# Kernel optimization log

Hardware: AMD Instinct MI355X
Metric: run time of the kernel (lower is better)

The kernel has to match this reference:

```python
import jax, jax.numpy as jnp
import numpy as np

N_AGENTS, OBS_DIM, HID, ACT_DIM = 8192, 64, 128, 16


def setup_inputs() -> dict:
    key = jax.random.key(0)
    k = jax.random.split(key, 8)
    obs_agents = jax.random.normal(k[0], (N_AGENTS, OBS_DIM), dtype=jnp.float32)
    # binary adjacency, {0,1}, int32 (index/mask semantics, non-differentiable)
    adj = jax.random.randint(k[1], (N_AGENTS, N_AGENTS), 0, 2, dtype=jnp.int32)
    def lin(kk, fan_in, fan_out):
        lim = 1.0 / np.sqrt(fan_in)
        kw, kb = jax.random.split(kk)
        W = jax.random.uniform(kw, (fan_in, fan_out), jnp.float32, -lim, lim)
        b = jax.random.uniform(kb, (fan_out,), jnp.float32, -lim, lim)
        return W, b
    W1, b1 = lin(k[2], OBS_DIM, HID)          # encoder
    W2, b2 = lin(k[3], 2 * HID, HID)          # actor layer 1
    W3, b3 = lin(k[4], HID, ACT_DIM)          # actor layer 2
    return {"obs_agents": obs_agents, "adj": adj,
            "W1": W1, "b1": b1, "W2": W2, "b2": b2, "W3": W3, "b3": b3}


def reference(obs_agents, adj, W1, b1, W2, b2, W3, b3):
    # per-agent encode: h = tanh(obs @ W1 + b1)  -> [N, HID]
    h = jnp.tanh(obs_agents @ W1 + b1)
    # neighbor mean message: mean of h[j] over j with adj[i,j]!=0, zeros if no neighbors
    a = adj.astype(h.dtype)                      # [N, N] binary
    deg = jnp.sum(a, axis=1, keepdims=True)      # [N, 1]
    msg = (a @ h) / jnp.maximum(deg, 1.0)        # zero rows stay zero
    # actor MLP on concat([h, msg])
    combined = jnp.concatenate([h, msg], axis=-1)            # [N, 2*HID]
    hid = jnp.tanh(combined @ W2 + b2)                        # [N, HID]
    logits = hid @ W3 + b3                                    # [N, ACT_DIM]
    return logits
```

## Files before the change

### kernel.cpp

```cpp
#include <hip/hip_runtime.h>
#include <stdint.h>
#include <math.h>

#define NAG 8192
#define NB  144
#define BM  64
#define LDA 72
#define LDB 72
#define NSPLIT 8

typedef __attribute__((ext_vector_type(8))) short short8;
typedef __attribute__((ext_vector_type(4))) float floatx4;

__device__ __forceinline__ float bf2f(unsigned short u) {
    union { uint32_t i; float f; } v; v.i = ((uint32_t)u) << 16; return v.f;
}
__device__ __forceinline__ unsigned short f2bf(float f) {
    union { float f; uint32_t i; } v; v.f = f;
    uint32_t x = v.i;
    return (unsigned short)((x + 0x7FFFu + ((x >> 16) & 1u)) >> 16);
}
__device__ __forceinline__ unsigned short f2h(float f) {
    union { _Float16 h; unsigned short u; } v; v.h = (_Float16)f; return v.u;
}
__device__ __forceinline__ float h2f(unsigned short u) {
    union { _Float16 h; unsigned short u; } v; v.u = u; return (float)v.h;
}

__global__ __launch_bounds__(64) void k0_init(
    int* __restrict__ flag, const unsigned short* __restrict__ W1raw)
{
    int big = 0;
    #pragma unroll
    for (int j = 0; j < 8; ++j) {
        float v = bf2f(W1raw[threadIdx.x * 8 + j]);
        if (!(fabsf(v) <= 1e6f)) big = 1;
    }
    unsigned long long m = __ballot(big);
    if (threadIdx.x == 0) *flag = (m != 0ull) ? 1 : 0;
}

__global__ __launch_bounds__(256) void k1_encode(
    const void* __restrict__ obs,
    const void* __restrict__ W1,
    const void* __restrict__ b1,
    const int* __restrict__ flag,
    float* __restrict__ h_f32,
    unsigned short* __restrict__ hT)
{
    __shared__ float obs_lds[32][68];
    __shared__ unsigned short ht_lds[128][33];
    const int t = threadIdx.x;
    const int abase = blockIdx.x * 32;
    const bool isf = (*flag != 0);

    {
        int a = t >> 3, c0 = (t & 7) * 8;
        if (isf) {
            const float* p = (const float*)obs;
            #pragma unroll
            for (int j = 0; j < 8; ++j)
                obs_lds[a][c0 + j] = p[(size_t)(abase + a) * 64 + c0 + j];
        } else {
            const unsigned short* p = (const unsigned short*)obs;
            #pragma unroll
            for (int j = 0; j < 8; ++j)
                obs_lds[a][c0 + j] = bf2f(p[(size_t)(abase + a) * 64 + c0 + j]);
        }
    }
    __syncthreads();

    const int o = t & 127;
    const int half = t >> 7;
    float acc[16];
    if (isf) {
        const float* Wp = (const float*)W1;
        float bias = ((const float*)b1)[o];
        #pragma unroll
        for (int i = 0; i < 16; ++i) acc[i] = bias;
        for (int k0 = 0; k0 < 64; k0 += 8) {
            float w[8];
            #pragma unroll
            for (int j = 0; j < 8; ++j) w[j] = Wp[(k0 + j) * 128 + o];
            #pragma unroll
            for (int j = 0; j < 8; ++j)
                #pragma unroll
                for (int i = 0; i < 16; ++i)
                    acc[i] = fmaf(obs_lds[half * 16 + i][k0 + j], w[j], acc[i]);
        }
    } else {
        const unsigned short* Wp = (const unsigned short*)W1;
        float bias = bf2f(((const unsigned short*)b1)[o]);
        #pragma unroll
        for (int i = 0; i < 16; ++i) acc[i] = bias;
        for (int k0 = 0; k0 < 64; k0 += 8) {
            float w[8];
            #pragma unroll
            for (int j = 0; j < 8; ++j) w[j] = bf2f(Wp[(k0 + j) * 128 + o]);
            #pragma unroll
            for (int j = 0; j < 8; ++j)
                #pragma unroll
                for (int i = 0; i < 16; ++i)
                    acc[i] = fmaf(obs_lds[half * 16 + i][k0 + j], w[j], acc[i]);
        }
    }
    #pragma unroll
    for (int i = 0; i < 16; ++i) {
        float th = tanhf(acc[i]);
        int a = half * 16 + i;
        h_f32[(size_t)(abase + a) * 128 + o] = th;
        ht_lds[o][a] = f2bf(th);
    }
    __syncthreads();

    for (int p = 0; p < 18; ++p) {
        int n = p * 8 + (t >> 5);
        int a = t & 31;
        unsigned short v;
        if (n < 128)       v = ht_lds[n][a];
        else if (n == 128) v = 0x3F80;
        else               v = 0;
        hT[(size_t)n * NAG + abase + a] = v;
    }
}

__global__ __launch_bounds__(256, 4) void k2_msggemm(
    const int* __restrict__ adj,
    const unsigned short* __restrict__ hT,
    unsigned short* __restrict__ Cp16)
{
    __shared__ __align__(16) unsigned short Alds[BM * LDA];
    __shared__ __align__(16) unsigned short Blds[NB * LDB];
    const int t = threadIdx.x;
    const int mtile = blockIdx.x & 127;
    const int ks = blockIdx.x >> 7;
    const int row0 = mtile * BM;
    const int kbeg = ks * 1024;

    const int wave = t >> 6, lane = t & 63;
    const int fm = lane & 15, quad = lane >> 4;

    floatx4 acc[9];
    #pragma unroll
    for (int i = 0; i < 9; ++i) acc[i] = (floatx4)0.f;

    const int ar = t >> 2, aq = t & 3;
    const int bln = t & 7, brow = t >> 3;

    const int* aP = adj + (size_t)(row0 + ar) * NAG + aq * 16;
    int4 rA0[4], rA1[4];
    uint4 rB[5];

#define LOADA(R, K) do { \
        _Pragma("unroll") \
        for (int c = 0; c < 4; ++c) \
            (R)[c] = *reinterpret_cast<const int4*>(aP + (K) + c * 4); \
    } while (0)
#define LOADB(K) do { \
        _Pragma("unroll") \
        for (int p = 0; p < 5; ++p) { \
            int n = p * 32 + brow; \
            if (n < NB) rB[p] = *reinterpret_cast<const uint4*>(hT + (size_t)n * NAG + (K) + bln * 8); \
        } \
    } while (0)
#define STOREA(R) do { \
        _Pragma("unroll") \
        for (int c = 0; c < 4; ++c) { \
            uint32_t d0 = ((uint32_t)(R)[c].x | ((uint32_t)(R)[c].y << 16)) * 0x3F80u; \
            uint32_t d1 = ((uint32_t)(R)[c].z | ((uint32_t)(R)[c].w << 16)) * 0x3F80u; \
            *reinterpret_cast<uint2*>(&Alds[ar * LDA + aq * 16 + c * 4]) = make_uint2(d0, d1); \
        } \
    } while (0)
#define STOREB() do { \
        _Pragma("unroll") \
        for (int p = 0; p < 5; ++p) { \
            int n = p * 32 + brow; \
            if (n < NB) *reinterpret_cast<uint4*>(&Blds[n * LDB + bln * 8]) = rB[p]; \
        } \
    } while (0)
#define COMPUTE() do { \
        _Pragma("unroll") \
        for (int kk = 0; kk < 64; kk += 32) { \
            short8 af = *reinterpret_cast<const short8*>(&Alds[(wave * 16 + fm) * LDA + kk + quad * 8]); \
            _Pragma("unroll") \
            for (int j = 0; j < 9; ++j) { \
                short8 bf = *reinterpret_cast<const short8*>(&Blds[(j * 16 + fm) * LDB + kk + quad * 8]); \
                acc[j] = __builtin_amdgcn_mfma_f32_16x16x32_bf16(af, bf, acc[j], 0, 0, 0); \
            } \
        } \
    } while (0)

    LOADA(rA0, kbeg);
    LOADA(rA1, kbeg + 64);
    LOADB(kbeg);

    for (int it = 0; it < 16; it += 2) {
        __syncthreads();
        STOREA(rA0);
        STOREB();
        __syncthreads();
        if (it + 1 < 16) LOADB(kbeg + (it + 1) * 64);
        if (it + 2 < 16) LOADA(rA0, kbeg + (it + 2) * 64);
        COMPUTE();
        __syncthreads();
        STOREA(rA1);
        STOREB();
        __syncthreads();
        if (it + 2 < 16) LOADB(kbeg + (it + 2) * 64);
        if (it + 3 < 16) LOADA(rA1, kbeg + (it + 3) * 64);
        COMPUTE();
    }

    unsigned short* out = Cp16 + (size_t)ks * (NAG * NB);
    #pragma unroll
    for (int j = 0; j < 9; ++j) {
        int col = j * 16 + fm;
        #pragma unroll
        for (int r = 0; r < 4; ++r) {
            int row = row0 + wave * 16 + quad * 4 + r;
            out[(size_t)row * NB + col] = f2h(acc[j][r]);
        }
    }
#undef LOADA
#undef LOADB
#undef STOREA
#undef STOREB
#undef COMPUTE
}

__global__ __launch_bounds__(256) void k3_actor(
    const float* __restrict__ h_f32,
    const unsigned short* __restrict__ Cp16,
    const void* __restrict__ W2,
    const void* __restrict__ b2,
    const void* __restrict__ W3,
    const void* __restrict__ b3,
    const int* __restrict__ flag,
    void* __restrict__ out)
{
    __shared__ float4 comb4[16][66];
    __shared__ float hid[16][132];
    __shared__ float inv_lds[16];
    const int t = threadIdx.x;
    const int abase = blockIdx.x * 16;
    const bool isf = (*flag != 0);
    const size_t PS = (size_t)NAG * NB;

    if (t < 16) {
        float deg = 0.f;
        #pragma unroll
        for (int s = 0; s < NSPLIT; ++s)
            deg += h2f(Cp16[s * PS + (size_t)(abase + t) * NB + 128]);
        inv_lds[t] = 1.0f / fmaxf(deg, 1.0f);
    }
    __syncthreads();

    #pragma unroll
    for (int jj = 0; jj < 4; ++jj) {
        int idx = jj * 256 + t;
        int a = idx >> 6, q = idx & 63;
        float4 v;
        if (q < 32) {
            v = *reinterpret_cast<const float4*>(h_f32 + (size_t)(abase + a) * 128 + q * 4);
        } else {
            int f = (q - 32) * 4;
            float s0 = 0.f, s1 = 0.f, s2 = 0.f, s3 = 0.f;
            #pragma unroll
            for (int s = 0; s < NSPLIT; ++s) {
                ushort4 p = *reinterpret_cast<const ushort4*>(Cp16 + s * PS + (size_t)(abase + a) * NB + f);
                s0 += h2f(p.x); s1 += h2f(p.y); s2 += h2f(p.z); s3 += h2f(p.w);
            }
            float sc = inv_lds[a];
            v = make_float4(s0 * sc, s1 * sc, s2 * sc, s3 * sc);
        }
        comb4[a][q] = v;
    }
    __syncthreads();

    const int o = t & 127, half = t >> 7;
    float acc[8];
    if (isf) {
        const float* Wp = (const float*)W2;
        float bias = ((const float*)b2)[o];
        #pragma unroll
        for (int i = 0; i < 8; ++i) acc[i] = bias;
        for (int cq = 0; cq < 64; ++cq) {
            float w0 = Wp[(cq * 4 + 0) * 128 + o];
            float w1 = Wp[(cq * 4 + 1) * 128 + o];
            float w2 = Wp[(cq * 4 + 2) * 128 + o];
            float w3 = Wp[(cq * 4 + 3) * 128 + o];
            #pragma unroll
            for (int i = 0; i < 8; ++i) {
                float4 v = comb4[half * 8 + i][cq];
                acc[i] = fmaf(v.x, w0, acc[i]);
                acc[i] = fmaf(v.y, w1, acc[i]);
                acc[i] = fmaf(v.z, w2, acc[i]);
                acc[i] = fmaf(v.w, w3, acc[i]);
            }
        }
    } else {
        const unsigned short* Wp = (const unsigned short*)W2;
        float bias = bf2f(((const unsigned short*)b2)[o]);
        #pragma unroll
        for (int i = 0; i < 8; ++i) acc[i] = bias;
        for (int cq = 0; cq < 64; ++cq) {
            float w0 = bf2f(Wp[(cq * 4 + 0) * 128 + o]);
            float w1 = bf2f(Wp[(cq * 4 + 1) * 128 + o]);
            float w2 = bf2f(Wp[(cq * 4 + 2) * 128 + o]);
            float w3 = bf2f(Wp[(cq * 4 + 3) * 128 + o]);
            #pragma unroll
            for (int i = 0; i < 8; ++i) {
                float4 v = comb4[half * 8 + i][cq];
                acc[i] = fmaf(v.x, w0, acc[i]);
                acc[i] = fmaf(v.y, w1, acc[i]);
                acc[i] = fmaf(v.z, w2, acc[i]);
                acc[i] = fmaf(v.w, w3, acc[i]);
            }
        }
    }
    #pragma unroll
    for (int i = 0; i < 8; ++i)
        hid[half * 8 + i][o] = tanhf(acc[i]);
    __syncthreads();

    const int q = t & 15, ar = t >> 4;
    float l;
    if (isf) {
        const float* Wp = (const float*)W3;
        l = ((const float*)b3)[q];
        #pragma unroll 4
        for (int oo = 0; oo < 128; ++oo)
            l = fmaf(hid[ar][oo], Wp[oo * 16 + q], l);
    } else {
        const unsigned short* Wp = (const unsigned short*)W3;
        l = bf2f(((const unsigned short*)b3)[q]);
        #pragma unroll 4
        for (int oo = 0; oo < 128; ++oo)
            l = fmaf(hid[ar][oo], bf2f(Wp[oo * 16 + q]), l);
    }
    size_t i0 = (size_t)(abase + ar) * 16 + q;
    if (isf) ((float*)out)[i0] = l;
    else     ((unsigned short*)out)[i0] = f2bf(l);
}

extern "C" void kernel_launch(void* const* d_in, const int* in_sizes, int n_in,
                              void* d_out, int out_size, void* d_ws, size_t ws_size,
                              hipStream_t stream) {
    const void* obs = d_in[0];
    const int*  adj = (const int*)d_in[1];
    const void* W1  = d_in[2];
    const void* b1  = d_in[3];
    const void* W2  = d_in[4];
    const void* b2  = d_in[5];
    const void* W3  = d_in[6];
    const void* b3  = d_in[7];

    char* ws = (char*)d_ws;
    unsigned short* hT   = (unsigned short*)(ws);
    float*          h_f32= (float*)(ws + 2359296);
    unsigned short* Cp16 = (unsigned short*)(ws + 6553600);
    int*            flag = (int*)(ws + 25427968);

    hipLaunchKernelGGL(k0_init, dim3(1), dim3(64), 0, stream, flag, (const unsigned short*)W1);
    hipLaunchKernelGGL(k1_encode, dim3(256), dim3(256), 0, stream, obs, W1, b1, flag, h_f32, hT);
    hipLaunchKernelGGL(k2_msggemm, dim3(1024), dim3(256), 0, stream, adj, hT, Cp16);
    hipLaunchKernelGGL(k3_actor, dim3(512), dim3(256), 0, stream, h_f32, Cp16, W2, b2, W3, b3, flag, d_out);
}
```

Measured before the change: 522.2 us.

## Load adjacency and hT tiles directly to LDS with XOR-swizzled layout

Replaces the register-staged, double-buffered global loads in the message GEMM with global_load_lds direct-to-LDS transfers. Raw int32 adjacency now sits in LDS and is converted to bf16 when fragments are read. Both tiles use an XOR swizzle instead of padding to avoid bank conflicts, and the constant degree/zero rows of hT are written once rather than loaded. The aim is to cut VGPR pressure and the register-to-LDS store traffic. The cost is a single-buffered loop with two barriers per 64-wide k-step and no prefetch overlap, and the A tile in LDS doubles in size.

```diff
diff --git a/kernel.cpp b/kernel.cpp
--- a/kernel.cpp
+++ b/kernel.cpp
@@ -5,8 +5,6 @@
 #define NAG 8192
 #define NB  144
 #define BM  64
-#define LDA 72
-#define LDB 72
 #define NSPLIT 8
 
 typedef __attribute__((ext_vector_type(8))) short short8;
@@ -25,6 +23,11 @@
 }
 __device__ __forceinline__ float h2f(unsigned short u) {
     union { _Float16 h; unsigned short u; } v; v.u = u; return (float)v.h;
+}
+__device__ __forceinline__ void gload_lds16(const void* g, void* lds) {
+    __builtin_amdgcn_global_load_lds(
+        (const __attribute__((address_space(1))) uint32_t*)g,
+        (__attribute__((address_space(3))) uint32_t*)lds, 16, 0, 0);
 }
 
 __global__ __launch_bounds__(64) void k0_init(
@@ -129,8 +132,8 @@
     const unsigned short* __restrict__ hT,
     unsigned short* __restrict__ Cp16)
 {
-    __shared__ __align__(16) unsigned short Alds[BM * LDA];
-    __shared__ __align__(16) unsigned short Blds[NB * LDB];
+    __shared__ __align__(16) int Alds[64 * 64];
+    __shared__ __align__(16) unsigned short Blds[144 * 64];
     const int t = threadIdx.x;
     const int mtile = blockIdx.x & 127;
     const int ks = blockIdx.x >> 7;
@@ -144,71 +147,64 @@
     #pragma unroll
     for (int i = 0; i < 9; ++i) acc[i] = (floatx4)0.f;
 
-    const int ar = t >> 2, aq = t & 3;
-    const int bln = t & 7, brow = t >> 3;
-
-    const int* aP = adj + (size_t)(row0 + ar) * NAG + aq * 16;
-    int4 rA0[4], rA1[4];
-    uint4 rB[5];
-
-#define LOADA(R, K) do { \
-        _Pragma("unroll") \
-        for (int c = 0; c < 4; ++c) \
-            (R)[c] = *reinterpret_cast<const int4*>(aP + (K) + c * 4); \
-    } while (0)
-#define LOADB(K) do { \
-        _Pragma("unroll") \
-        for (int p = 0; p < 5; ++p) { \
-            int n = p * 32 + brow; \
-            if (n < NB) rB[p] = *reinterpret_cast<const uint4*>(hT + (size_t)n * NAG + (K) + bln * 8); \
-        } \
-    } while (0)
-#define STOREA(R) do { \
-        _Pragma("unroll") \
-        for (int c = 0; c < 4; ++c) { \
-            uint32_t d0 = ((uint32_t)(R)[c].x | ((uint32_t)(R)[c].y << 16)) * 0x3F80u; \
-            uint32_t d1 = ((uint32_t)(R)[c].z | ((uint32_t)(R)[c].w << 16)) * 0x3F80u; \
-            *reinterpret_cast<uint2*>(&Alds[ar * LDA + aq * 16 + c * 4]) = make_uint2(d0, d1); \
-        } \
-    } while (0)
-#define STOREB() do { \
-        _Pragma("unroll") \
-        for (int p = 0; p < 5; ++p) { \
-            int n = p * 32 + brow; \
-            if (n < NB) *reinterpret_cast<uint4*>(&Blds[n * LDB + bln * 8]) = rB[p]; \
-        } \
-    } while (0)
-#define COMPUTE() do { \
-        _Pragma("unroll") \
-        for (int kk = 0; kk < 64; kk += 32) { \
-            short8 af = *reinterpret_cast<const short8*>(&Alds[(wave * 16 + fm) * LDA + kk + quad * 8]); \
-            _Pragma("unroll") \
-            for (int j = 0; j < 9; ++j) { \
-                short8 bf = *reinterpret_cast<const short8*>(&Blds[(j * 16 + fm) * LDB + kk + quad * 8]); \
-                acc[j] = __builtin_amdgcn_mfma_f32_16x16x32_bf16(af, bf, acc[j], 0, 0, 0); \
-            } \
-        } \
-    } while (0)
-
-    LOADA(rA0, kbeg);
-    LOADA(rA1, kbeg + 64);
-    LOADB(kbeg);
-
-    for (int it = 0; it < 16; it += 2) {
+    const int ra0 = 16 * wave + (lane >> 4);
+    const int* a0 = adj + (size_t)(row0 + ra0 +  0) * NAG + kbeg + (((lane & 15) ^ ((ra0 +  0) & 15)) << 2);
+    const int* a1 = adj + (size_t)(row0 + ra0 +  4) * NAG + kbeg + (((lane & 15) ^ ((ra0 +  4) & 15)) << 2);
+    const int* a2 = adj + (size_t)(row0 + ra0 +  8) * NAG + kbeg + (((lane & 15) ^ ((ra0 +  8) & 15)) << 2);
+    const int* a3 = adj + (size_t)(row0 + ra0 + 12) * NAG + kbeg + (((lane & 15) ^ ((ra0 + 12) & 15)) << 2);
+    const int rb0 = 32 * wave + (lane >> 3);
+    const int bco = (((lane & 7) ^ ((lane >> 3) & 7)) << 3);
+    const unsigned short* b0 = hT + (size_t)(rb0 +  0) * NAG + kbeg + bco;
+    const unsigned short* b1 = hT + (size_t)(rb0 +  8) * NAG + kbeg + bco;
+    const unsigned short* b2 = hT + (size_t)(rb0 + 16) * NAG + kbeg + bco;
+    const unsigned short* b3 = hT + (size_t)(rb0 + 24) * NAG + kbeg + bco;
+    int* Ad0 = &Alds[(wave * 4 + 0) * 256];
+    int* Ad1 = &Alds[(wave * 4 + 1) * 256];
+    int* Ad2 = &Alds[(wave * 4 + 2) * 256];
+    int* Ad3 = &Alds[(wave * 4 + 3) * 256];
+    unsigned short* Bd0 = &Blds[(wave * 4 + 0) * 512];
+    unsigned short* Bd1 = &Blds[(wave * 4 + 1) * 512];
+    unsigned short* Bd2 = &Blds[(wave * 4 + 2) * 512];
+    unsigned short* Bd3 = &Blds[(wave * 4 + 3) * 512];
+
+    {
+        int rr = 128 + (t >> 4);
+        int off = (t & 15) * 4;
+        uint32_t vv = (rr == 128) ? 0x3F803F80u : 0u;
+        *reinterpret_cast<uint2*>(&Blds[rr * 64 + off]) = make_uint2(vv, vv);
+    }
+
+    for (int it = 0; it < 16; ++it) {
+        const int ko = it * 64;
         __syncthreads();
-        STOREA(rA0);
-        STOREB();
+        gload_lds16(a0 + ko, Ad0);
+        gload_lds16(a1 + ko, Ad1);
+        gload_lds16(a2 + ko, Ad2);
+        gload_lds16(a3 + ko, Ad3);
+        gload_lds16(b0 + ko, Bd0);
+        gload_lds16(b1 + ko, Bd1);
+        gload_lds16(b2 + ko, Bd2);
+        gload_lds16(b3 + ko, Bd3);
         __syncthreads();
-        if (it + 1 < 16) LOADB(kbeg + (it + 1) * 64);
-        if (it + 2 < 16) LOADA(rA0, kbeg + (it + 2) * 64);
-        COMPUTE();
-        __syncthreads();
-        STOREA(rA1);
-        STOREB();
-        __syncthreads();
-        if (it + 2 < 16) LOADB(kbeg + (it + 2) * 64);
-        if (it + 3 < 16) LOADA(rA1, kbeg + (it + 3) * 64);
-        COMPUTE();
+        #pragma unroll
+        for (int kk = 0; kk < 64; kk += 32) {
+            const int arow = (wave * 16 + fm) * 64;
+            const int c0 = (kk >> 2) + 2 * quad;
+            int4 v0 = *reinterpret_cast<const int4*>(&Alds[arow + (((c0 + 0) ^ fm) << 2)]);
+            int4 v1 = *reinterpret_cast<const int4*>(&Alds[arow + (((c0 + 1) ^ fm) << 2)]);
+            union { uint32_t u[4]; short8 s; } af;
+            af.u[0] = ((uint32_t)v0.x | ((uint32_t)v0.y << 16)) * 0x3F80u;
+            af.u[1] = ((uint32_t)v0.z | ((uint32_t)v0.w << 16)) * 0x3F80u;
+            af.u[2] = ((uint32_t)v1.x | ((uint32_t)v1.y << 16)) * 0x3F80u;
+            af.u[3] = ((uint32_t)v1.z | ((uint32_t)v1.w << 16)) * 0x3F80u;
+            const int bc = (kk >> 3) + quad;
+            #pragma unroll
+            for (int j = 0; j < 9; ++j) {
+                int rb = j * 16 + fm;
+                short8 bf = *reinterpret_cast<const short8*>(&Blds[rb * 64 + ((bc ^ (fm & 7)) << 3)]);
+                acc[j] = __builtin_amdgcn_mfma_f32_16x16x32_bf16(af.s, bf, acc[j], 0, 0, 0);
+            }
+        }
     }
 
     unsigned short* out = Cp16 + (size_t)ks * (NAG * NB);
@@ -221,11 +217,6 @@
             out[(size_t)row * NB + col] = f2h(acc[j][r]);
         }
     }
-#undef LOADA
-#undef LOADB
-#undef STOREA
-#undef STOREB
-#undef COMPUTE
 }
 
 __global__ __launch_bounds__(256) void k3_actor(
```

Measured after the change: 467.0 us. 10.6% less time.
